# Performance work log

Hardware: AMD Instinct MI355X
Metric: run time of the kernel (lower is better)

## Reference

```python
import jax, jax.numpy as jnp
import numpy as np
import math

B, L, H, E = 4, 2048, 16, 64
S, D = L, E


def setup_inputs() -> dict:
    key = jax.random.key(0)
    kq, kk, kv = jax.random.split(key, 3)
    queries = jax.random.normal(kq, (B, L, H, E), dtype=jnp.float32)
    keys = jax.random.normal(kk, (B, S, H, E), dtype=jnp.float32)
    values = jax.random.normal(kv, (B, S, H, D), dtype=jnp.float32)
    # TriangularCausalMask: True above the diagonal => masked out
    attn_mask = jnp.broadcast_to(
        jnp.triu(jnp.ones((L, S), dtype=bool), k=1)[None, None], (B, 1, L, S)
    )
    return {"queries": queries, "keys": keys, "values": values, "attn_mask": attn_mask}


def reference(queries, keys, values, attn_mask):
    Edim = queries.shape[-1]
    scale = 1.0 / math.sqrt(Edim)  # self.scale is None -> 1/sqrt(E)
    # scores: [B, H, L, S]
    scores = jnp.einsum("blhe,bshe->bhls", queries, keys)
    # mask BEFORE scaling (as in original); -inf is invariant under positive scale
    scores = jnp.where(attn_mask, -jnp.inf, scores)
    attn = jax.nn.softmax(scale * scores, axis=-1)  # dropout p=0.0 -> identity
    out = jnp.einsum("bhls,bshd->blhd", attn, values)
    return out
```

## Files before the change

kernel.cpp:

```cpp
#include <hip/hip_runtime.h>


#define B_ 4
#define L_ 2048
#define H_ 16

typedef __attribute__((ext_vector_type(4))) float f32x4;
typedef __attribute__((ext_vector_type(8))) short bf16x8;

#if __has_builtin(__builtin_amdgcn_exp2f)
#define EXP2(x) __builtin_amdgcn_exp2f(x)
#else
#define EXP2(x) exp2f(x)
#endif

#if __has_builtin(__builtin_amdgcn_sched_barrier)
#define SCHED_FENCE() __builtin_amdgcn_sched_barrier(0)
#else
#define SCHED_FENCE()
#endif

__device__ __forceinline__ unsigned pkbf(float lo, float hi) {
    union { float f; unsigned u; } a, b;
    a.f = lo; b.f = hi;
    return __builtin_amdgcn_perm(b.u, a.u, 0x07060302u);
}

__global__ __launch_bounds__(256, 2) void attn_fwd(
    const float* __restrict__ Q, const float* __restrict__ K,
    const float* __restrict__ V, float* __restrict__ O)
{
    __shared__ unsigned smem[9216];

    const int tid = threadIdx.x;
    const int w   = tid >> 6;
    const int l   = tid & 63;
    const int l15 = l & 15;
    const int qd  = l >> 4;
    const int bh  = blockIdx.x & 63;
    const int pr  = blockIdx.x >> 6;
    const int b   = bh >> 4, h = bh & 15;
    const float cexp = 0.125f * 1.44269504088896340736f;

    const float* Kb = K + (((size_t)b * L_) * H_ + h) * 64;
    const float* Vb = V + (((size_t)b * L_) * H_ + h) * 64;

    const int krow = tid >> 2, kq = tid & 3;
    const int kmrow = (((krow >> 2) & 1) << 5) | (((krow >> 5) & 1) << 4)
                    | (((krow >> 3) & 3) << 2) | (krow & 3);
    const int vsp  = tid >> 3, vdg = tid & 7;
    const int vswz = vsp ^ (4 * vdg);

    for (int ph = 0; ph < 2; ++ph) {
        const int t    = ph ? pr : 15 - pr;
        const int qr0  = t * 128 + w * 32;
        const int mykb = (qr0 >> 6) + 1;
        const int nkb  = 2 * (t + 1);

        bf16x8 qf[2][2];
#pragma unroll
        for (int rt = 0; rt < 2; ++rt) {
            const int row = qr0 + 16 * rt + l15;
            const float* qp = Q + (((size_t)b * L_ + row) * H_ + h) * 64 + qd * 8;
#pragma unroll
            for (int ke = 0; ke < 2; ++ke) {
                float4 f0 = *(const float4*)(qp + ke * 32);
                float4 f1 = *(const float4*)(qp + ke * 32 + 4);
                union { unsigned u[4]; bf16x8 v; } cv;
                cv.u[0] = pkbf(f0.x * cexp, f0.y * cexp);
                cv.u[1] = pkbf(f0.z * cexp, f0.w * cexp);
                cv.u[2] = pkbf(f1.x * cexp, f1.y * cexp);
                cv.u[3] = pkbf(f1.z * cexp, f1.w * cexp);
                qf[rt][ke] = cv.v;
            }
        }

        f32x4 o[4][2];
#pragma unroll
        for (int dt = 0; dt < 4; ++dt)
#pragma unroll
            for (int rt = 0; rt < 2; ++rt)
                o[dt][rt] = (f32x4){0.f, 0.f, 0.f, 0.f};
        float ls[2] = {0.f, 0.f};

        {
            const float* kg = Kb + (size_t)krow * 1024 + kq * 16;
            float4 k0 = *(const float4*)(kg + 0);
            float4 k1 = *(const float4*)(kg + 4);
            float4 k2 = *(const float4*)(kg + 8);
            float4 k3 = *(const float4*)(kg + 12);
            const float* vg = Vb + (size_t)(2 * vsp) * 1024 + vdg * 8;
            float4 v0 = *(const float4*)(vg + 0);
            float4 v1 = *(const float4*)(vg + 4);
            float4 v2 = *(const float4*)(vg + 1024);
            float4 v3 = *(const float4*)(vg + 1028);
            unsigned* kd = smem + kmrow * 36 + kq * 8;
            uint4 w0, w1;
            w0.x = pkbf(k0.x, k0.y); w0.y = pkbf(k0.z, k0.w);
            w0.z = pkbf(k1.x, k1.y); w0.w = pkbf(k1.z, k1.w);
            w1.x = pkbf(k2.x, k2.y); w1.y = pkbf(k2.z, k2.w);
            w1.z = pkbf(k3.x, k3.y); w1.w = pkbf(k3.z, k3.w);
            *(uint4*)kd = w0;
            *(uint4*)(kd + 4) = w1;
            unsigned* vd = smem + 2304 + (8 * vdg) * 36 + vswz;
            vd[0 * 36] = pkbf(v0.x, v2.x);
            vd[1 * 36] = pkbf(v0.y, v2.y);
            vd[2 * 36] = pkbf(v0.z, v2.z);
            vd[3 * 36] = pkbf(v0.w, v2.w);
            vd[4 * 36] = pkbf(v1.x, v3.x);
            vd[5 * 36] = pkbf(v1.y, v3.y);
            vd[6 * 36] = pkbf(v1.z, v3.z);
            vd[7 * 36] = pkbf(v1.w, v3.w);
        }
        __syncthreads();

        for (int kb = 0; kb < nkb; ++kb) {
            const bool more = (kb + 1 < nkb);
            float4 nk0, nk1, nk2, nk3, nv0, nv1, nv2, nv3;
            if (more) {
                const float* kg = Kb + (size_t)((kb + 1) * 64 + krow) * 1024 + kq * 16;
                nk0 = *(const float4*)(kg + 0);
                nk1 = *(const float4*)(kg + 4);
                nk2 = *(const float4*)(kg + 8);
                nk3 = *(const float4*)(kg + 12);
                const float* vg = Vb + (size_t)((kb + 1) * 64 + 2 * vsp) * 1024 + vdg * 8;
                nv0 = *(const float4*)(vg + 0);
                nv1 = *(const float4*)(vg + 4);
                nv2 = *(const float4*)(vg + 1024);
                nv3 = *(const float4*)(vg + 1028);
            }

            if (kb < mykb) {
                const unsigned* Kl = smem + (kb & 1) * 4608;
                const unsigned* Vl = Kl + 2304;

                f32x4 st[4][2];
#pragma unroll
                for (int kt = 0; kt < 4; ++kt)
#pragma unroll
                    for (int rt = 0; rt < 2; ++rt)
                        st[kt][rt] = (f32x4){0.f, 0.f, 0.f, 0.f};
#pragma unroll
                for (int kt = 0; kt < 4; ++kt)
#pragma unroll
                    for (int ke = 0; ke < 2; ++ke) {
                        bf16x8 a = *(const bf16x8*)(Kl + (kt * 16 + l15) * 36 + ke * 16 + qd * 4);
                        st[kt][0] = __builtin_amdgcn_mfma_f32_16x16x32_bf16(a, qf[0][ke], st[kt][0], 0, 0, 0);
                        st[kt][1] = __builtin_amdgcn_mfma_f32_16x16x32_bf16(a, qf[1][ke], st[kt][1], 0, 0, 0);
                    }

                if (kb == mykb - 1) {
#pragma unroll
                    for (int kt = 0; kt < 4; ++kt)
#pragma unroll
                        for (int rt = 0; rt < 2; ++rt) {
                            const int rowg = qr0 + 16 * rt + l15;
#pragma unroll
                            for (int r = 0; r < 4; ++r) {
                                const int key = kb * 64 + (kt & 1) * 32 + qd * 8
                                              + (kt >> 1) * 4 + r;
                                if (key > rowg) st[kt][rt][r] = -1e30f;
                            }
                        }
                }

                float sacc0 = 0.f, sacc1 = 0.f;
#pragma unroll
                for (int kt = 0; kt < 4; ++kt)
#pragma unroll
                    for (int r = 0; r < 4; ++r) {
                        float p0 = EXP2(st[kt][0][r]);
                        float p1 = EXP2(st[kt][1][r]);
                        st[kt][0][r] = p0;
                        st[kt][1][r] = p1;
                        sacc0 += p0;
                        sacc1 += p1;
                    }
                ls[0] += sacc0;
                ls[1] += sacc1;

                bf16x8 vf[2][4];
#pragma unroll
                for (int se = 0; se < 2; ++se)
#pragma unroll
                    for (int dt = 0; dt < 4; ++dt) {
                        const int col = (se * 16 + qd * 4) ^ (4 * (2 * dt + (l15 >> 3)));
                        vf[se][dt] = *(const bf16x8*)(Vl + (dt * 16 + l15) * 36 + col);
                    }

#pragma unroll
                for (int se = 0; se < 2; ++se)
#pragma unroll
                    for (int rt = 0; rt < 2; ++rt) {
                        union { unsigned u[4]; bf16x8 v; } pb;
                        pb.u[0] = pkbf(st[se][rt][0], st[se][rt][1]);
                        pb.u[1] = pkbf(st[se][rt][2], st[se][rt][3]);
                        pb.u[2] = pkbf(st[se + 2][rt][0], st[se + 2][rt][1]);
                        pb.u[3] = pkbf(st[se + 2][rt][2], st[se + 2][rt][3]);
#pragma unroll
                        for (int dt = 0; dt < 4; ++dt)
                            o[dt][rt] = __builtin_amdgcn_mfma_f32_16x16x32_bf16(vf[se][dt], pb.v, o[dt][rt], 0, 0, 0);
                    }
            }

            if (more) {
                SCHED_FENCE();
                unsigned* bK = smem + ((kb + 1) & 1) * 4608;
                unsigned* kd = bK + kmrow * 36 + kq * 8;
                uint4 w0, w1;
                w0.x = pkbf(nk0.x, nk0.y); w0.y = pkbf(nk0.z, nk0.w);
                w0.z = pkbf(nk1.x, nk1.y); w0.w = pkbf(nk1.z, nk1.w);
                w1.x = pkbf(nk2.x, nk2.y); w1.y = pkbf(nk2.z, nk2.w);
                w1.z = pkbf(nk3.x, nk3.y); w1.w = pkbf(nk3.z, nk3.w);
                *(uint4*)kd = w0;
                *(uint4*)(kd + 4) = w1;
                unsigned* vd = bK + 2304 + (8 * vdg) * 36 + vswz;
                vd[0 * 36] = pkbf(nv0.x, nv2.x);
                vd[1 * 36] = pkbf(nv0.y, nv2.y);
                vd[2 * 36] = pkbf(nv0.z, nv2.z);
                vd[3 * 36] = pkbf(nv0.w, nv2.w);
                vd[4 * 36] = pkbf(nv1.x, nv3.x);
                vd[5 * 36] = pkbf(nv1.y, nv3.y);
                vd[6 * 36] = pkbf(nv1.z, nv3.z);
                vd[7 * 36] = pkbf(nv1.w, nv3.w);
                __syncthreads();
            }
        }

#pragma unroll
        for (int rt = 0; rt < 2; ++rt) {
            float s = ls[rt];
            s += __shfl_xor(s, 16);
            s += __shfl_xor(s, 32);
            const float inv = 1.0f / s;
            const int row = qr0 + 16 * rt + l15;
            float* op = O + (((size_t)b * L_ + row) * H_ + h) * 64 + qd * 4;
#pragma unroll
            for (int dt = 0; dt < 4; ++dt) {
                float4 wv;
                wv.x = o[dt][rt][0] * inv;
                wv.y = o[dt][rt][1] * inv;
                wv.z = o[dt][rt][2] * inv;
                wv.w = o[dt][rt][3] * inv;
                *(float4*)(op + dt * 16) = wv;
            }
        }
        if (ph == 0) __syncthreads();
    }
}

extern "C" void kernel_launch(void* const* d_in, const int* in_sizes, int n_in,
                              void* d_out, int out_size, void* d_ws, size_t ws_size,
                              hipStream_t stream) {
    const float* Q = (const float*)d_in[0];
    const float* K = (const float*)d_in[1];
    const float* V = (const float*)d_in[2];
    float* O = (float*)d_out;

    dim3 grid(64 * 8);
    dim3 block(256);
    hipLaunchKernelGGL(attn_fwd, grid, block, 0, stream, Q, K, V, O);
}
```

Baseline: 208.1 us.

## Run both causal query tiles concurrently in a 512-thread block sharing K/V loads

```diff
diff --git a/kernel.cpp b/kernel.cpp
--- a/kernel.cpp
+++ b/kernel.cpp
@@ -26,7 +26,7 @@
     return __builtin_amdgcn_perm(b.u, a.u, 0x07060302u);
 }
 
-__global__ __launch_bounds__(256, 2) void attn_fwd(
+__global__ __launch_bounds__(512, 2) void attn_fwd(
     const float* __restrict__ Q, const float* __restrict__ K,
     const float* __restrict__ V, float* __restrict__ O)
 {
@@ -38,214 +38,192 @@
     const int l15 = l & 15;
     const int qd  = l >> 4;
     const int bh  = blockIdx.x & 63;
-    const int pr  = blockIdx.x >> 6;
+    const int pg  = blockIdx.x >> 6;
+    const int pr  = (pg < 4) ? pg : 11 - pg;
     const int b   = bh >> 4, h = bh & 15;
     const float cexp = 0.125f * 1.44269504088896340736f;
 
     const float* Kb = K + (((size_t)b * L_) * H_ + h) * 64;
     const float* Vb = V + (((size_t)b * L_) * H_ + h) * 64;
 
-    const int krow = tid >> 2, kq = tid & 3;
+    const int t    = (w < 4) ? (15 - pr) : pr;
+    const int qr0  = t * 128 + (w & 3) * 32;
+    const int mykb = (qr0 >> 6) + 1;
+    const int nkb  = 2 * (16 - pr);
+
+    const int krow = tid >> 3, kq = tid & 7;
     const int kmrow = (((krow >> 2) & 1) << 5) | (((krow >> 5) & 1) << 4)
                     | (((krow >> 3) & 3) << 2) | (krow & 3);
-    const int vsp  = tid >> 3, vdg = tid & 7;
+    const int vsp = tid >> 4;
+    const int vdg = (tid >> 1) & 7;
+    const int vh  = tid & 1;
     const int vswz = vsp ^ (4 * vdg);
 
-    for (int ph = 0; ph < 2; ++ph) {
-        const int t    = ph ? pr : 15 - pr;
-        const int qr0  = t * 128 + w * 32;
-        const int mykb = (qr0 >> 6) + 1;
-        const int nkb  = 2 * (t + 1);
-
-        bf16x8 qf[2][2];
-#pragma unroll
-        for (int rt = 0; rt < 2; ++rt) {
-            const int row = qr0 + 16 * rt + l15;
-            const float* qp = Q + (((size_t)b * L_ + row) * H_ + h) * 64 + qd * 8;
-#pragma unroll
-            for (int ke = 0; ke < 2; ++ke) {
-                float4 f0 = *(const float4*)(qp + ke * 32);
-                float4 f1 = *(const float4*)(qp + ke * 32 + 4);
-                union { unsigned u[4]; bf16x8 v; } cv;
-                cv.u[0] = pkbf(f0.x * cexp, f0.y * cexp);
-                cv.u[1] = pkbf(f0.z * cexp, f0.w * cexp);
-                cv.u[2] = pkbf(f1.x * cexp, f1.y * cexp);
-                cv.u[3] = pkbf(f1.z * cexp, f1.w * cexp);
-                qf[rt][ke] = cv.v;
-            }
-        }
-
-        f32x4 o[4][2];
-#pragma unroll
-        for (int dt = 0; dt < 4; ++dt)
-#pragma unroll
-            for (int rt = 0; rt < 2; ++rt)
-                o[dt][rt] = (f32x4){0.f, 0.f, 0.f, 0.f};
-        float ls[2] = {0.f, 0.f};
-
-        {
-            const float* kg = Kb + (size_t)krow * 1024 + kq * 16;
-            float4 k0 = *(const float4*)(kg + 0);
-            float4 k1 = *(const float4*)(kg + 4);
-            float4 k2 = *(const float4*)(kg + 8);
-            float4 k3 = *(const float4*)(kg + 12);
-            const float* vg = Vb + (size_t)(2 * vsp) * 1024 + vdg * 8;
-            float4 v0 = *(const float4*)(vg + 0);
-            float4 v1 = *(const float4*)(vg + 4);
-            float4 v2 = *(const float4*)(vg + 1024);
-            float4 v3 = *(const float4*)(vg + 1028);
-            unsigned* kd = smem + kmrow * 36 + kq * 8;
-            uint4 w0, w1;
-            w0.x = pkbf(k0.x, k0.y); w0.y = pkbf(k0.z, k0.w);
-            w0.z = pkbf(k1.x, k1.y); w0.w = pkbf(k1.z, k1.w);
-            w1.x = pkbf(k2.x, k2.y); w1.y = pkbf(k2.z, k2.w);
-            w1.z = pkbf(k3.x, k3.y); w1.w = pkbf(k3.z, k3.w);
-            *(uint4*)kd = w0;
-            *(uint4*)(kd + 4) = w1;
-            unsigned* vd = smem + 2304 + (8 * vdg) * 36 + vswz;
-            vd[0 * 36] = pkbf(v0.x, v2.x);
-            vd[1 * 36] = pkbf(v0.y, v2.y);
-            vd[2 * 36] = pkbf(v0.z, v2.z);
-            vd[3 * 36] = pkbf(v0.w, v2.w);
-            vd[4 * 36] = pkbf(v1.x, v3.x);
-            vd[5 * 36] = pkbf(v1.y, v3.y);
-            vd[6 * 36] = pkbf(v1.z, v3.z);
-            vd[7 * 36] = pkbf(v1.w, v3.w);
-        }
-        __syncthreads();
-
-        for (int kb = 0; kb < nkb; ++kb) {
-            const bool more = (kb + 1 < nkb);
-            float4 nk0, nk1, nk2, nk3, nv0, nv1, nv2, nv3;
-            if (more) {
-                const float* kg = Kb + (size_t)((kb + 1) * 64 + krow) * 1024 + kq * 16;
-                nk0 = *(const float4*)(kg + 0);
-                nk1 = *(const float4*)(kg + 4);
-                nk2 = *(const float4*)(kg + 8);
-                nk3 = *(const float4*)(kg + 12);
-                const float* vg = Vb + (size_t)((kb + 1) * 64 + 2 * vsp) * 1024 + vdg * 8;
-                nv0 = *(const float4*)(vg + 0);
-                nv1 = *(const float4*)(vg + 4);
-                nv2 = *(const float4*)(vg + 1024);
-                nv3 = *(const float4*)(vg + 1028);
-            }
-
-            if (kb < mykb) {
-                const unsigned* Kl = smem + (kb & 1) * 4608;
-                const unsigned* Vl = Kl + 2304;
-
-                f32x4 st[4][2];
+    bf16x8 qf[2][2];
+#pragma unroll
+    for (int rt = 0; rt < 2; ++rt) {
+        const int row = qr0 + 16 * rt + l15;
+        const float* qp = Q + (((size_t)b * L_ + row) * H_ + h) * 64 + qd * 8;
+#pragma unroll
+        for (int ke = 0; ke < 2; ++ke) {
+            float4 f0 = *(const float4*)(qp + ke * 32);
+            float4 f1 = *(const float4*)(qp + ke * 32 + 4);
+            union { unsigned u[4]; bf16x8 v; } cv;
+            cv.u[0] = pkbf(f0.x * cexp, f0.y * cexp);
+            cv.u[1] = pkbf(f0.z * cexp, f0.w * cexp);
+            cv.u[2] = pkbf(f1.x * cexp, f1.y * cexp);
+            cv.u[3] = pkbf(f1.z * cexp, f1.w * cexp);
+            qf[rt][ke] = cv.v;
+        }
+    }
+
+    f32x4 o[4][2];
+#pragma unroll
+    for (int dt = 0; dt < 4; ++dt)
+#pragma unroll
+        for (int rt = 0; rt < 2; ++rt)
+            o[dt][rt] = (f32x4){0.f, 0.f, 0.f, 0.f};
+    float ls[2] = {0.f, 0.f};
+
+    {
+        const float* kg = Kb + (size_t)krow * 1024 + kq * 8;
+        float4 k0 = *(const float4*)(kg + 0);
+        float4 k1 = *(const float4*)(kg + 4);
+        const float* vg = Vb + (size_t)(2 * vsp) * 1024 + vdg * 8 + vh * 4;
+        float4 v0 = *(const float4*)(vg + 0);
+        float4 v1 = *(const float4*)(vg + 1024);
+        unsigned* kd = smem + kmrow * 36 + kq * 4;
+        uint4 w0;
+        w0.x = pkbf(k0.x, k0.y); w0.y = pkbf(k0.z, k0.w);
+        w0.z = pkbf(k1.x, k1.y); w0.w = pkbf(k1.z, k1.w);
+        *(uint4*)kd = w0;
+        unsigned* vd = smem + 2304 + (8 * vdg + 4 * vh) * 36 + vswz;
+        vd[0 * 36] = pkbf(v0.x, v1.x);
+        vd[1 * 36] = pkbf(v0.y, v1.y);
+        vd[2 * 36] = pkbf(v0.z, v1.z);
+        vd[3 * 36] = pkbf(v0.w, v1.w);
+    }
+    __syncthreads();
+
+    for (int kb = 0; kb < nkb; ++kb) {
+        const bool more = (kb + 1 < nkb);
+        float4 nk0, nk1, nv0, nv1;
+        if (more) {
+            const float* kg = Kb + (size_t)((kb + 1) * 64 + krow) * 1024 + kq * 8;
+            nk0 = *(const float4*)(kg + 0);
+            nk1 = *(const float4*)(kg + 4);
+            const float* vg = Vb + (size_t)((kb + 1) * 64 + 2 * vsp) * 1024 + vdg * 8 + vh * 4;
+            nv0 = *(const float4*)(vg + 0);
+            nv1 = *(const float4*)(vg + 1024);
+        }
+
+        if (kb < mykb) {
+            const unsigned* Kl = smem + (kb & 1) * 4608;
+            const unsigned* Vl = Kl + 2304;
+
+            f32x4 st[4][2];
+#pragma unroll
+            for (int kt = 0; kt < 4; ++kt)
+#pragma unroll
+                for (int rt = 0; rt < 2; ++rt)
+                    st[kt][rt] = (f32x4){0.f, 0.f, 0.f, 0.f};
+#pragma unroll
+            for (int kt = 0; kt < 4; ++kt)
+#pragma unroll
+                for (int ke = 0; ke < 2; ++ke) {
+                    bf16x8 a = *(const bf16x8*)(Kl + (kt * 16 + l15) * 36 + ke * 16 + qd * 4);
+                    st[kt][0] = __builtin_amdgcn_mfma_f32_16x16x32_bf16(a, qf[0][ke], st[kt][0], 0, 0, 0);
+                    st[kt][1] = __builtin_amdgcn_mfma_f32_16x16x32_bf16(a, qf[1][ke], st[kt][1], 0, 0, 0);
+                }
+
+            if (kb == mykb - 1) {
 #pragma unroll
                 for (int kt = 0; kt < 4; ++kt)
 #pragma unroll
-                    for (int rt = 0; rt < 2; ++rt)
-                        st[kt][rt] = (f32x4){0.f, 0.f, 0.f, 0.f};
-#pragma unroll
-                for (int kt = 0; kt < 4; ++kt)
-#pragma unroll
-                    for (int ke = 0; ke < 2; ++ke) {
-                        bf16x8 a = *(const bf16x8*)(Kl + (kt * 16 + l15) * 36 + ke * 16 + qd * 4);
-                        st[kt][0] = __builtin_amdgcn_mfma_f32_16x16x32_bf16(a, qf[0][ke], st[kt][0], 0, 0, 0);
-                        st[kt][1] = __builtin_amdgcn_mfma_f32_16x16x32_bf16(a, qf[1][ke], st[kt][1], 0, 0, 0);
-                    }
-
-                if (kb == mykb - 1) {
-#pragma unroll
-                    for (int kt = 0; kt < 4; ++kt)
-#pragma unroll
-                        for (int rt = 0; rt < 2; ++rt) {
-                            const int rowg = qr0 + 16 * rt + l15;
-#pragma unroll
-                            for (int r = 0; r < 4; ++r) {
-                                const int key = kb * 64 + (kt & 1) * 32 + qd * 8
-                                              + (kt >> 1) * 4 + r;
-                                if (key > rowg) st[kt][rt][r] = -1e30f;
-                            }
+                    for (int rt = 0; rt < 2; ++rt) {
+                        const int rowg = qr0 + 16 * rt + l15;
+#pragma unroll
+                        for (int r = 0; r < 4; ++r) {
+                            const int key = kb * 64 + (kt & 1) * 32 + qd * 8
+                                          + (kt >> 1) * 4 + r;
+                            if (key > rowg) st[kt][rt][r] = -1e30f;
                         }
-                }
-
-                float sacc0 = 0.f, sacc1 = 0.f;
-#pragma unroll
-                for (int kt = 0; kt < 4; ++kt)
-#pragma unroll
-                    for (int r = 0; r < 4; ++r) {
-                        float p0 = EXP2(st[kt][0][r]);
-                        float p1 = EXP2(st[kt][1][r]);
-                        st[kt][0][r] = p0;
-                        st[kt][1][r] = p1;
-                        sacc0 += p0;
-                        sacc1 += p1;
-                    }
-                ls[0] += sacc0;
-                ls[1] += sacc1;
-
-                bf16x8 vf[2][4];
-#pragma unroll
-                for (int se = 0; se < 2; ++se)
-#pragma unroll
-                    for (int dt = 0; dt < 4; ++dt) {
-                        const int col = (se * 16 + qd * 4) ^ (4 * (2 * dt + (l15 >> 3)));
-                        vf[se][dt] = *(const bf16x8*)(Vl + (dt * 16 + l15) * 36 + col);
-                    }
-
-#pragma unroll
-                for (int se = 0; se < 2; ++se)
-#pragma unroll
-                    for (int rt = 0; rt < 2; ++rt) {
-                        union { unsigned u[4]; bf16x8 v; } pb;
-                        pb.u[0] = pkbf(st[se][rt][0], st[se][rt][1]);
-                        pb.u[1] = pkbf(st[se][rt][2], st[se][rt][3]);
-                        pb.u[2] = pkbf(st[se + 2][rt][0], st[se + 2][rt][1]);
-                        pb.u[3] = pkbf(st[se + 2][rt][2], st[se + 2][rt][3]);
-#pragma unroll
-                        for (int dt = 0; dt < 4; ++dt)
-                            o[dt][rt] = __builtin_amdgcn_mfma_f32_16x16x32_bf16(vf[se][dt], pb.v, o[dt][rt], 0, 0, 0);
                     }
             }
 
-            if (more) {
-                SCHED_FENCE();
-                unsigned* bK = smem + ((kb + 1) & 1) * 4608;
-                unsigned* kd = bK + kmrow * 36 + kq * 8;
-                uint4 w0, w1;
-                w0.x = pkbf(nk0.x, nk0.y); w0.y = pkbf(nk0.z, nk0.w);
-                w0.z = pkbf(nk1.x, nk1.y); w0.w = pkbf(nk1.z, nk1.w);
-                w1.x = pkbf(nk2.x, nk2.y); w1.y = pkbf(nk2.z, nk2.w);
-                w1.z = pkbf(nk3.x, nk3.y); w1.w = pkbf(nk3.z, nk3.w);
-                *(uint4*)kd = w0;
-                *(uint4*)(kd + 4) = w1;
-                unsigned* vd = bK + 2304 + (8 * vdg) * 36 + vswz;
-                vd[0 * 36] = pkbf(nv0.x, nv2.x);
-                vd[1 * 36] = pkbf(nv0.y, nv2.y);
-                vd[2 * 36] = pkbf(nv0.z, nv2.z);
-                vd[3 * 36] = pkbf(nv0.w, nv2.w);
-                vd[4 * 36] = pkbf(nv1.x, nv3.x);
-                vd[5 * 36] = pkbf(nv1.y, nv3.y);
-                vd[6 * 36] = pkbf(nv1.z, nv3.z);
-                vd[7 * 36] = pkbf(nv1.w, nv3.w);
-                __syncthreads();
-            }
-        }
-
-#pragma unroll
-        for (int rt = 0; rt < 2; ++rt) {
-            float s = ls[rt];
-            s += __shfl_xor(s, 16);
-            s += __shfl_xor(s, 32);
-            const float inv = 1.0f / s;
-            const int row = qr0 + 16 * rt + l15;
-            float* op = O + (((size_t)b * L_ + row) * H_ + h) * 64 + qd * 4;
-#pragma unroll
-            for (int dt = 0; dt < 4; ++dt) {
-                float4 wv;
-                wv.x = o[dt][rt][0] * inv;
-                wv.y = o[dt][rt][1] * inv;
-                wv.z = o[dt][rt][2] * inv;
-                wv.w = o[dt][rt][3] * inv;
-                *(float4*)(op + dt * 16) = wv;
-            }
-        }
-        if (ph == 0) __syncthreads();
+            float sacc0 = 0.f, sacc1 = 0.f;
+#pragma unroll
+            for (int kt = 0; kt < 4; ++kt)
+#pragma unroll
+                for (int r = 0; r < 4; ++r) {
+                    float p0 = EXP2(st[kt][0][r]);
+                    float p1 = EXP2(st[kt][1][r]);
+                    st[kt][0][r] = p0;
+                    st[kt][1][r] = p1;
+                    sacc0 += p0;
+                    sacc1 += p1;
+                }
+            ls[0] += sacc0;
+            ls[1] += sacc1;
+
+            bf16x8 vf[2][4];
+#pragma unroll
+            for (int se = 0; se < 2; ++se)
+#pragma unroll
+                for (int dt = 0; dt < 4; ++dt) {
+                    const int col = (se * 16 + qd * 4) ^ (4 * (2 * dt + (l15 >> 3)));
+                    vf[se][dt] = *(const bf16x8*)(Vl + (dt * 16 + l15) * 36 + col);
+                }
+
+#pragma unroll
+            for (int se = 0; se < 2; ++se)
+#pragma unroll
+                for (int rt = 0; rt < 2; ++rt) {
+                    union { unsigned u[4]; bf16x8 v; } pb;
+                    pb.u[0] = pkbf(st[se][rt][0], st[se][rt][1]);
+                    pb.u[1] = pkbf(st[se][rt][2], st[se][rt][3]);
+                    pb.u[2] = pkbf(st[se + 2][rt][0], st[se + 2][rt][1]);
+                    pb.u[3] = pkbf(st[se + 2][rt][2], st[se + 2][rt][3]);
+#pragma unroll
+                    for (int dt = 0; dt < 4; ++dt)
+                        o[dt][rt] = __builtin_amdgcn_mfma_f32_16x16x32_bf16(vf[se][dt], pb.v, o[dt][rt], 0, 0, 0);
+                }
+        }
+
+        if (more) {
+            SCHED_FENCE();
+            unsigned* bK = smem + ((kb + 1) & 1) * 4608;
+            unsigned* kd = bK + kmrow * 36 + kq * 4;
+            uint4 w0;
+            w0.x = pkbf(nk0.x, nk0.y); w0.y = pkbf(nk0.z, nk0.w);
+            w0.z = pkbf(nk1.x, nk1.y); w0.w = pkbf(nk1.z, nk1.w);
+            *(uint4*)kd = w0;
+            unsigned* vd = bK + 2304 + (8 * vdg + 4 * vh) * 36 + vswz;
+            vd[0 * 36] = pkbf(nv0.x, nv1.x);
+            vd[1 * 36] = pkbf(nv0.y, nv1.y);
+            vd[2 * 36] = pkbf(nv0.z, nv1.z);
+            vd[3 * 36] = pkbf(nv0.w, nv1.w);
+            __syncthreads();
+        }
+    }
+
+#pragma unroll
+    for (int rt = 0; rt < 2; ++rt) {
+        float s = ls[rt];
+        s += __shfl_xor(s, 16);
+        s += __shfl_xor(s, 32);
+        const float inv = 1.0f / s;
+        const int row = qr0 + 16 * rt + l15;
+        float* op = O + (((size_t)b * L_ + row) * H_ + h) * 64 + qd * 4;
+#pragma unroll
+        for (int dt = 0; dt < 4; ++dt) {
+            float4 wv;
+            wv.x = o[dt][rt][0] * inv;
+            wv.y = o[dt][rt][1] * inv;
+            wv.z = o[dt][rt][2] * inv;
+            wv.w = o[dt][rt][3] * inv;
+            *(float4*)(op + dt * 16) = wv;
+        }
     }
 }
 
@@ -258,6 +236,6 @@
     float* O = (float*)d_out;
 
     dim3 grid(64 * 8);
-    dim3 block(256);
+    dim3 block(512);
     hipLaunchKernelGGL(attn_fwd, grid, block, 0, stream, Q, K, V, O);
 }
```

Measured after the change: 220.0 us. 5.7% more time.

## Use 256-row query tiles per block instead of paired causal tiles

Applied to the files above, without the earlier changes.

```diff
diff --git a/kernel.cpp b/kernel.cpp
--- a/kernel.cpp
+++ b/kernel.cpp
@@ -20,6 +20,13 @@
 #define SCHED_FENCE()
 #endif
 
+#define BAR() do {                                              \
+    SCHED_FENCE();                                              \
+    asm volatile("s_waitcnt lgkmcnt(0)" ::: "memory");          \
+    __builtin_amdgcn_s_barrier();                               \
+    SCHED_FENCE();                                              \
+} while (0)
+
 __device__ __forceinline__ unsigned pkbf(float lo, float hi) {
     union { float f; unsigned u; } a, b;
     a.f = lo; b.f = hi;
@@ -34,16 +41,20 @@
 
     const int tid = threadIdx.x;
     const int w   = tid >> 6;
-    const int l   = tid & 63;
-    const int l15 = l & 15;
-    const int qd  = l >> 4;
+    const int l15 = tid & 15;
+    const int qd  = (tid >> 4) & 3;
     const int bh  = blockIdx.x & 63;
-    const int pr  = blockIdx.x >> 6;
+    const int g   = blockIdx.x >> 6;
+    const int u   = (g < 4) ? g : 11 - g;
     const int b   = bh >> 4, h = bh & 15;
     const float cexp = 0.125f * 1.44269504088896340736f;
 
     const float* Kb = K + (((size_t)b * L_) * H_ + h) * 64;
     const float* Vb = V + (((size_t)b * L_) * H_ + h) * 64;
+
+    const int qr0  = u * 256 + w * 64;
+    const int mykb = 4 * u + w + 1;
+    const int nkb  = 4 * u + 4;
 
     const int krow = tid >> 2, kq = tid & 3;
     const int kmrow = (((krow >> 2) & 1) << 5) | (((krow >> 5) & 1) << 4)
@@ -51,201 +62,223 @@
     const int vsp  = tid >> 3, vdg = tid & 7;
     const int vswz = vsp ^ (4 * vdg);
 
-    for (int ph = 0; ph < 2; ++ph) {
-        const int t    = ph ? pr : 15 - pr;
-        const int qr0  = t * 128 + w * 32;
-        const int mykb = (qr0 >> 6) + 1;
-        const int nkb  = 2 * (t + 1);
-
-        bf16x8 qf[2][2];
-#pragma unroll
-        for (int rt = 0; rt < 2; ++rt) {
-            const int row = qr0 + 16 * rt + l15;
-            const float* qp = Q + (((size_t)b * L_ + row) * H_ + h) * 64 + qd * 8;
-#pragma unroll
-            for (int ke = 0; ke < 2; ++ke) {
-                float4 f0 = *(const float4*)(qp + ke * 32);
-                float4 f1 = *(const float4*)(qp + ke * 32 + 4);
-                union { unsigned u[4]; bf16x8 v; } cv;
-                cv.u[0] = pkbf(f0.x * cexp, f0.y * cexp);
-                cv.u[1] = pkbf(f0.z * cexp, f0.w * cexp);
-                cv.u[2] = pkbf(f1.x * cexp, f1.y * cexp);
-                cv.u[3] = pkbf(f1.z * cexp, f1.w * cexp);
-                qf[rt][ke] = cv.v;
+    bf16x8 qf[4][2];
+#pragma unroll
+    for (int rt = 0; rt < 4; ++rt) {
+        const int row = qr0 + 16 * rt + l15;
+        const float* qp = Q + (((size_t)b * L_ + row) * H_ + h) * 64 + qd * 8;
+#pragma unroll
+        for (int ke = 0; ke < 2; ++ke) {
+            float4 f0 = *(const float4*)(qp + ke * 32);
+            float4 f1 = *(const float4*)(qp + ke * 32 + 4);
+            union { unsigned uu[4]; bf16x8 v; } cv;
+            cv.uu[0] = pkbf(f0.x * cexp, f0.y * cexp);
+            cv.uu[1] = pkbf(f0.z * cexp, f0.w * cexp);
+            cv.uu[2] = pkbf(f1.x * cexp, f1.y * cexp);
+            cv.uu[3] = pkbf(f1.z * cexp, f1.w * cexp);
+            qf[rt][ke] = cv.v;
+        }
+    }
+
+    f32x4 o[4][4];
+#pragma unroll
+    for (int dt = 0; dt < 4; ++dt)
+#pragma unroll
+        for (int rt = 0; rt < 4; ++rt)
+            o[dt][rt] = (f32x4){0.f, 0.f, 0.f, 0.f};
+    float ls[4] = {0.f, 0.f, 0.f, 0.f};
+
+    {
+        const float* kg = Kb + (size_t)krow * 1024 + kq * 16;
+        float4 k0 = *(const float4*)(kg + 0);
+        float4 k1 = *(const float4*)(kg + 4);
+        float4 k2 = *(const float4*)(kg + 8);
+        float4 k3 = *(const float4*)(kg + 12);
+        const float* vg = Vb + (size_t)(2 * vsp) * 1024 + vdg * 8;
+        float4 v0 = *(const float4*)(vg + 0);
+        float4 v1 = *(const float4*)(vg + 4);
+        float4 v2 = *(const float4*)(vg + 1024);
+        float4 v3 = *(const float4*)(vg + 1028);
+        unsigned* kd = smem + kmrow * 36 + kq * 8;
+        uint4 w0, w1;
+        w0.x = pkbf(k0.x, k0.y); w0.y = pkbf(k0.z, k0.w);
+        w0.z = pkbf(k1.x, k1.y); w0.w = pkbf(k1.z, k1.w);
+        w1.x = pkbf(k2.x, k2.y); w1.y = pkbf(k2.z, k2.w);
+        w1.z = pkbf(k3.x, k3.y); w1.w = pkbf(k3.z, k3.w);
+        *(uint4*)kd = w0;
+        *(uint4*)(kd + 4) = w1;
+        unsigned* vd = smem + 2304 + (8 * vdg) * 36 + vswz;
+        vd[0 * 36] = pkbf(v0.x, v2.x);
+        vd[1 * 36] = pkbf(v0.y, v2.y);
+        vd[2 * 36] = pkbf(v0.z, v2.z);
+        vd[3 * 36] = pkbf(v0.w, v2.w);
+        vd[4 * 36] = pkbf(v1.x, v3.x);
+        vd[5 * 36] = pkbf(v1.y, v3.y);
+        vd[6 * 36] = pkbf(v1.z, v3.z);
+        vd[7 * 36] = pkbf(v1.w, v3.w);
+    }
+    BAR();
+
+    for (int kb = 0; kb < nkb; ++kb) {
+        const bool more = (kb + 1 < nkb);
+        float4 nk0, nk1, nk2, nk3, nv0, nv1, nv2, nv3;
+        if (more) {
+            const float* kg = Kb + (size_t)((kb + 1) * 64 + krow) * 1024 + kq * 16;
+            nk0 = *(const float4*)(kg + 0);
+            nk1 = *(const float4*)(kg + 4);
+            nk2 = *(const float4*)(kg + 8);
+            nk3 = *(const float4*)(kg + 12);
+            const float* vg = Vb + (size_t)((kb + 1) * 64 + 2 * vsp) * 1024 + vdg * 8;
+            nv0 = *(const float4*)(vg + 0);
+            nv1 = *(const float4*)(vg + 4);
+            nv2 = *(const float4*)(vg + 1024);
+            nv3 = *(const float4*)(vg + 1028);
+        }
+
+        if (kb < mykb) {
+            const unsigned* Kl = smem + (kb & 1) * 4608;
+            const unsigned* Vl = Kl + 2304;
+
+            f32x4 st0[4][2], st1[4][2];
+#pragma unroll
+            for (int kt = 0; kt < 4; ++kt)
+#pragma unroll
+                for (int rt = 0; rt < 2; ++rt) {
+                    st0[kt][rt] = (f32x4){0.f, 0.f, 0.f, 0.f};
+                    st1[kt][rt] = (f32x4){0.f, 0.f, 0.f, 0.f};
+                }
+            __builtin_amdgcn_s_setprio(1);
+#pragma unroll
+            for (int kt = 0; kt < 4; ++kt)
+#pragma unroll
+                for (int ke = 0; ke < 2; ++ke) {
+                    bf16x8 a = *(const bf16x8*)(Kl + (kt * 16 + l15) * 36 + ke * 16 + qd * 4);
+                    st0[kt][0] = __builtin_amdgcn_mfma_f32_16x16x32_bf16(a, qf[0][ke], st0[kt][0], 0, 0, 0);
+                    st0[kt][1] = __builtin_amdgcn_mfma_f32_16x16x32_bf16(a, qf[1][ke], st0[kt][1], 0, 0, 0);
+                    st1[kt][0] = __builtin_amdgcn_mfma_f32_16x16x32_bf16(a, qf[2][ke], st1[kt][0], 0, 0, 0);
+                    st1[kt][1] = __builtin_amdgcn_mfma_f32_16x16x32_bf16(a, qf[3][ke], st1[kt][1], 0, 0, 0);
+                }
+            __builtin_amdgcn_s_setprio(0);
+
+            if (kb == mykb - 1) {
+#pragma unroll
+                for (int kt = 0; kt < 4; ++kt)
+#pragma unroll
+                    for (int rt = 0; rt < 2; ++rt) {
+                        const int rowg0 = qr0 + 16 * rt + l15;
+                        const int rowg1 = qr0 + 16 * (rt + 2) + l15;
+#pragma unroll
+                        for (int r = 0; r < 4; ++r) {
+                            const int key = kb * 64 + (kt & 1) * 32 + qd * 8
+                                          + (kt >> 1) * 4 + r;
+                            if (key > rowg0) st0[kt][rt][r] = -1e30f;
+                            if (key > rowg1) st1[kt][rt][r] = -1e30f;
+                        }
+                    }
             }
-        }
-
-        f32x4 o[4][2];
-#pragma unroll
-        for (int dt = 0; dt < 4; ++dt)
+
+            float sa0 = 0.f, sa1 = 0.f, sa2 = 0.f, sa3 = 0.f;
+#pragma unroll
+            for (int kt = 0; kt < 4; ++kt)
+#pragma unroll
+                for (int r = 0; r < 4; ++r) {
+                    float p0 = EXP2(st0[kt][0][r]);
+                    float p1 = EXP2(st0[kt][1][r]);
+                    float p2 = EXP2(st1[kt][0][r]);
+                    float p3 = EXP2(st1[kt][1][r]);
+                    st0[kt][0][r] = p0;
+                    st0[kt][1][r] = p1;
+                    st1[kt][0][r] = p2;
+                    st1[kt][1][r] = p3;
+                    sa0 += p0; sa1 += p1; sa2 += p2; sa3 += p3;
+                }
+            ls[0] += sa0; ls[1] += sa1; ls[2] += sa2; ls[3] += sa3;
+
+            bf16x8 pbv[4][2];
 #pragma unroll
             for (int rt = 0; rt < 2; ++rt)
-                o[dt][rt] = (f32x4){0.f, 0.f, 0.f, 0.f};
-        float ls[2] = {0.f, 0.f};
-
-        {
-            const float* kg = Kb + (size_t)krow * 1024 + kq * 16;
-            float4 k0 = *(const float4*)(kg + 0);
-            float4 k1 = *(const float4*)(kg + 4);
-            float4 k2 = *(const float4*)(kg + 8);
-            float4 k3 = *(const float4*)(kg + 12);
-            const float* vg = Vb + (size_t)(2 * vsp) * 1024 + vdg * 8;
-            float4 v0 = *(const float4*)(vg + 0);
-            float4 v1 = *(const float4*)(vg + 4);
-            float4 v2 = *(const float4*)(vg + 1024);
-            float4 v3 = *(const float4*)(vg + 1028);
-            unsigned* kd = smem + kmrow * 36 + kq * 8;
+#pragma unroll
+                for (int se = 0; se < 2; ++se) {
+                    union { unsigned uu[4]; bf16x8 v; } pb;
+                    pb.uu[0] = pkbf(st0[se][rt][0], st0[se][rt][1]);
+                    pb.uu[1] = pkbf(st0[se][rt][2], st0[se][rt][3]);
+                    pb.uu[2] = pkbf(st0[se + 2][rt][0], st0[se + 2][rt][1]);
+                    pb.uu[3] = pkbf(st0[se + 2][rt][2], st0[se + 2][rt][3]);
+                    pbv[rt][se] = pb.v;
+                }
+#pragma unroll
+            for (int rt = 0; rt < 2; ++rt)
+#pragma unroll
+                for (int se = 0; se < 2; ++se) {
+                    union { unsigned uu[4]; bf16x8 v; } pb;
+                    pb.uu[0] = pkbf(st1[se][rt][0], st1[se][rt][1]);
+                    pb.uu[1] = pkbf(st1[se][rt][2], st1[se][rt][3]);
+                    pb.uu[2] = pkbf(st1[se + 2][rt][0], st1[se + 2][rt][1]);
+                    pb.uu[3] = pkbf(st1[se + 2][rt][2], st1[se + 2][rt][3]);
+                    pbv[2 + rt][se] = pb.v;
+                }
+
+            bf16x8 vf[2][4];
+#pragma unroll
+            for (int se = 0; se < 2; ++se)
+#pragma unroll
+                for (int dt = 0; dt < 4; ++dt) {
+                    const int col = (se * 16 + qd * 4) ^ (4 * (2 * dt + (l15 >> 3)));
+                    vf[se][dt] = *(const bf16x8*)(Vl + (dt * 16 + l15) * 36 + col);
+                }
+
+            __builtin_amdgcn_s_setprio(1);
+#pragma unroll
+            for (int se = 0; se < 2; ++se)
+#pragma unroll
+                for (int rt = 0; rt < 4; ++rt)
+#pragma unroll
+                    for (int dt = 0; dt < 4; ++dt)
+                        o[dt][rt] = __builtin_amdgcn_mfma_f32_16x16x32_bf16(vf[se][dt], pbv[rt][se], o[dt][rt], 0, 0, 0);
+            __builtin_amdgcn_s_setprio(0);
+        }
+
+        if (more) {
+            SCHED_FENCE();
+            unsigned* bK = smem + ((kb + 1) & 1) * 4608;
+            unsigned* kd = bK + kmrow * 36 + kq * 8;
             uint4 w0, w1;
-            w0.x = pkbf(k0.x, k0.y); w0.y = pkbf(k0.z, k0.w);
-            w0.z = pkbf(k1.x, k1.y); w0.w = pkbf(k1.z, k1.w);
-            w1.x = pkbf(k2.x, k2.y); w1.y = pkbf(k2.z, k2.w);
-            w1.z = pkbf(k3.x, k3.y); w1.w = pkbf(k3.z, k3.w);
+            w0.x = pkbf(nk0.x, nk0.y); w0.y = pkbf(nk0.z, nk0.w);
+            w0.z = pkbf(nk1.x, nk1.y); w0.w = pkbf(nk1.z, nk1.w);
+            w1.x = pkbf(nk2.x, nk2.y); w1.y = pkbf(nk2.z, nk2.w);
+            w1.z = pkbf(nk3.x, nk3.y); w1.w = pkbf(nk3.z, nk3.w);
             *(uint4*)kd = w0;
             *(uint4*)(kd + 4) = w1;
-            unsigned* vd = smem + 2304 + (8 * vdg) * 36 + vswz;
-            vd[0 * 36] = pkbf(v0.x, v2.x);
-            vd[1 * 36] = pkbf(v0.y, v2.y);
-            vd[2 * 36] = pkbf(v0.z, v2.z);
-            vd[3 * 36] = pkbf(v0.w, v2.w);
-            vd[4 * 36] = pkbf(v1.x, v3.x);
-            vd[5 * 36] = pkbf(v1.y, v3.y);
-            vd[6 * 36] = pkbf(v1.z, v3.z);
-            vd[7 * 36] = pkbf(v1.w, v3.w);
-        }
-        __syncthreads();
-
-        for (int kb = 0; kb < nkb; ++kb) {
-            const bool more = (kb + 1 < nkb);
-            float4 nk0, nk1, nk2, nk3, nv0, nv1, nv2, nv3;
-            if (more) {
-                const float* kg = Kb + (size_t)((kb + 1) * 64 + krow) * 1024 + kq * 16;
-                nk0 = *(const float4*)(kg + 0);
-                nk1 = *(const float4*)(kg + 4);
-                nk2 = *(const float4*)(kg + 8);
-                nk3 = *(const float4*)(kg + 12);
-                const float* vg = Vb + (size_t)((kb + 1) * 64 + 2 * vsp) * 1024 + vdg * 8;
-                nv0 = *(const float4*)(vg + 0);
-                nv1 = *(const float4*)(vg + 4);
-                nv2 = *(const float4*)(vg + 1024);
-                nv3 = *(const float4*)(vg + 1028);
-            }
-
-            if (kb < mykb) {
-                const unsigned* Kl = smem + (kb & 1) * 4608;
-                const unsigned* Vl = Kl + 2304;
-
-                f32x4 st[4][2];
-#pragma unroll
-                for (int kt = 0; kt < 4; ++kt)
-#pragma unroll
-                    for (int rt = 0; rt < 2; ++rt)
-                        st[kt][rt] = (f32x4){0.f, 0.f, 0.f, 0.f};
-#pragma unroll
-                for (int kt = 0; kt < 4; ++kt)
-#pragma unroll
-                    for (int ke = 0; ke < 2; ++ke) {
-                        bf16x8 a = *(const bf16x8*)(Kl + (kt * 16 + l15) * 36 + ke * 16 + qd * 4);
-                        st[kt][0] = __builtin_amdgcn_mfma_f32_16x16x32_bf16(a, qf[0][ke], st[kt][0], 0, 0, 0);
-                        st[kt][1] = __builtin_amdgcn_mfma_f32_16x16x32_bf16(a, qf[1][ke], st[kt][1], 0, 0, 0);
-                    }
-
-                if (kb == mykb - 1) {
-#pragma unroll
-                    for (int kt = 0; kt < 4; ++kt)
-#pragma unroll
-                        for (int rt = 0; rt < 2; ++rt) {
-                            const int rowg = qr0 + 16 * rt + l15;
-#pragma unroll
-                            for (int r = 0; r < 4; ++r) {
-                                const int key = kb * 64 + (kt & 1) * 32 + qd * 8
-                                              + (kt >> 1) * 4 + r;
-                                if (key > rowg) st[kt][rt][r] = -1e30f;
-                            }
-                        }
-                }
-
-                float sacc0 = 0.f, sacc1 = 0.f;
-#pragma unroll
-                for (int kt = 0; kt < 4; ++kt)
-#pragma unroll
-                    for (int r = 0; r < 4; ++r) {
-                        float p0 = EXP2(st[kt][0][r]);
-                        float p1 = EXP2(st[kt][1][r]);
-                        st[kt][0][r] = p0;
-                        st[kt][1][r] = p1;
-                        sacc0 += p0;
-                        sacc1 += p1;
-                    }
-                ls[0] += sacc0;
-                ls[1] += sacc1;
-
-                bf16x8 vf[2][4];
-#pragma unroll
-                for (int se = 0; se < 2; ++se)
-#pragma unroll
-                    for (int dt = 0; dt < 4; ++dt) {
-                        const int col = (se * 16 + qd * 4) ^ (4 * (2 * dt + (l15 >> 3)));
-                        vf[se][dt] = *(const bf16x8*)(Vl + (dt * 16 + l15) * 36 + col);
-                    }
-
-#pragma unroll
-                for (int se = 0; se < 2; ++se)
-#pragma unroll
-                    for (int rt = 0; rt < 2; ++rt) {
-                        union { unsigned u[4]; bf16x8 v; } pb;
-                        pb.u[0] = pkbf(st[se][rt][0], st[se][rt][1]);
-                        pb.u[1] = pkbf(st[se][rt][2], st[se][rt][3]);
-                        pb.u[2] = pkbf(st[se + 2][rt][0], st[se + 2][rt][1]);
-                        pb.u[3] = pkbf(st[se + 2][rt][2], st[se + 2][rt][3]);
-#pragma unroll
-                        for (int dt = 0; dt < 4; ++dt)
-                            o[dt][rt] = __builtin_amdgcn_mfma_f32_16x16x32_bf16(vf[se][dt], pb.v, o[dt][rt], 0, 0, 0);
-                    }
-            }
-
-            if (more) {
-                SCHED_FENCE();
-                unsigned* bK = smem + ((kb + 1) & 1) * 4608;
-                unsigned* kd = bK + kmrow * 36 + kq * 8;
-                uint4 w0, w1;
-                w0.x = pkbf(nk0.x, nk0.y); w0.y = pkbf(nk0.z, nk0.w);
-                w0.z = pkbf(nk1.x, nk1.y); w0.w = pkbf(nk1.z, nk1.w);
-                w1.x = pkbf(nk2.x, nk2.y); w1.y = pkbf(nk2.z, nk2.w);
-                w1.z = pkbf(nk3.x, nk3.y); w1.w = pkbf(nk3.z, nk3.w);
-                *(uint4*)kd = w0;
-                *(uint4*)(kd + 4) = w1;
-                unsigned* vd = bK + 2304 + (8 * vdg) * 36 + vswz;
-                vd[0 * 36] = pkbf(nv0.x, nv2.x);
-                vd[1 * 36] = pkbf(nv0.y, nv2.y);
-                vd[2 * 36] = pkbf(nv0.z, nv2.z);
-                vd[3 * 36] = pkbf(nv0.w, nv2.w);
-                vd[4 * 36] = pkbf(nv1.x, nv3.x);
-                vd[5 * 36] = pkbf(nv1.y, nv3.y);
-                vd[6 * 36] = pkbf(nv1.z, nv3.z);
-                vd[7 * 36] = pkbf(nv1.w, nv3.w);
-                __syncthreads();
-            }
-        }
-
-#pragma unroll
-        for (int rt = 0; rt < 2; ++rt) {
-            float s = ls[rt];
-            s += __shfl_xor(s, 16);
-            s += __shfl_xor(s, 32);
-            const float inv = 1.0f / s;
-            const int row = qr0 + 16 * rt + l15;
-            float* op = O + (((size_t)b * L_ + row) * H_ + h) * 64 + qd * 4;
-#pragma unroll
-            for (int dt = 0; dt < 4; ++dt) {
-                float4 wv;
-                wv.x = o[dt][rt][0] * inv;
-                wv.y = o[dt][rt][1] * inv;
-                wv.z = o[dt][rt][2] * inv;
-                wv.w = o[dt][rt][3] * inv;
-                *(float4*)(op + dt * 16) = wv;
-            }
-        }
-        if (ph == 0) __syncthreads();
+            unsigned* vd = bK + 2304 + (8 * vdg) * 36 + vswz;
+            vd[0 * 36] = pkbf(nv0.x, nv2.x);
+            vd[1 * 36] = pkbf(nv0.y, nv2.y);
+            vd[2 * 36] = pkbf(nv0.z, nv2.z);
+            vd[3 * 36] = pkbf(nv0.w, nv2.w);
+            vd[4 * 36] = pkbf(nv1.x, nv3.x);
+            vd[5 * 36] = pkbf(nv1.y, nv3.y);
+            vd[6 * 36] = pkbf(nv1.z, nv3.z);
+            vd[7 * 36] = pkbf(nv1.w, nv3.w);
+            BAR();
+        }
+    }
+
+#pragma unroll
+    for (int rt = 0; rt < 4; ++rt) {
+        float s = ls[rt];
+        s += __shfl_xor(s, 16);
+        s += __shfl_xor(s, 32);
+        const float inv = 1.0f / s;
+        const int row = qr0 + 16 * rt + l15;
+        float* op = O + (((size_t)b * L_ + row) * H_ + h) * 64 + qd * 4;
+#pragma unroll
+        for (int dt = 0; dt < 4; ++dt) {
+            float4 wv;
+            wv.x = o[dt][rt][0] * inv;
+            wv.y = o[dt][rt][1] * inv;
+            wv.z = o[dt][rt][2] * inv;
+            wv.w = o[dt][rt][3] * inv;
+            *(float4*)(op + dt * 16) = wv;
+        }
     }
 }
 
```

Result: slower. 230.0 us (+10.5%).
